# Kernel optimization log

Hardware: AMD Instinct MI355X
Metric: run time of the kernel (lower is better)

The kernel has to match this reference:

```python
import jax, jax.numpy as jnp
import numpy as np

D_MODEL = 2048
D_INNER = 2 * D_MODEL      # expand=2
D_STATE = 16
D_CONV = 4
DT_RANK = D_MODEL // 16    # ceil(2048/16)=128
BATCH, SEQLEN = 2, 1024


def setup_inputs() -> dict:
    key = jax.random.key(0)
    ks = jax.random.split(key, 10)
    s = 0.02
    inp = {
        "hidden_states": jax.random.normal(ks[0], (BATCH, SEQLEN, D_MODEL), jnp.float32),
        "in_proj_w": jax.random.normal(ks[1], (2 * D_INNER, D_MODEL), jnp.float32) * s,
        "conv_w": jax.random.normal(ks[2], (D_INNER, D_CONV), jnp.float32) * s,
        "conv_b": jax.random.normal(ks[3], (D_INNER,), jnp.float32) * s,
        "x_proj_w": jax.random.normal(ks[4], (DT_RANK + 2 * D_STATE, D_INNER), jnp.float32) * s,
        "dt_proj_w": jax.random.normal(ks[5], (D_INNER, DT_RANK), jnp.float32) * s,
        "dt_proj_b": jax.random.normal(ks[6], (D_INNER,), jnp.float32) * 0.1,
        "A_log": jnp.log(jnp.tile(jnp.arange(1, D_STATE + 1, dtype=jnp.float32), (D_INNER, 1))),
        "D": jnp.ones((D_INNER,), jnp.float32),
        "out_proj_w": jax.random.normal(ks[7], (D_MODEL, D_INNER), jnp.float32) * s,
    }
    return inp


def _mamba_forward(hidden_states, in_proj_w, conv_w, conv_b, x_proj_w,
                   dt_proj_w, dt_proj_b, A_log, D, out_proj_w):
    B, L, _ = hidden_states.shape
    # input projection -> x, z  (each [B, L, D_INNER])
    xz = jnp.einsum('bld,ed->ble', hidden_states, in_proj_w)
    x, z = jnp.split(xz, 2, axis=-1)
    # causal depthwise conv1d (kernel D_CONV) + SiLU
    x_pad = jnp.pad(x, ((0, 0), (D_CONV - 1, 0), (0, 0)))
    windows = jnp.stack([x_pad[:, k:k + L, :] for k in range(D_CONV)], axis=-1)  # [B,L,D,K]
    x_conv = jnp.einsum('bldk,dk->bld', windows, conv_w) + conv_b
    x_act = jax.nn.silu(x_conv)
    # data-dependent SSM parameters
    x_dbl = jnp.einsum('bld,ed->ble', x_act, x_proj_w)
    dt, Bc, Cc = jnp.split(x_dbl, [DT_RANK, DT_RANK + D_STATE], axis=-1)
    dt = jax.nn.softplus(jnp.einsum('blr,dr->bld', dt, dt_proj_w) + dt_proj_b)  # [B,L,D_INNER]
    A = -jnp.exp(A_log)  # [D_INNER, D_STATE]

    # selective scan over time (carry h: [B, D_INNER, D_STATE])
    def step(h, inp):
        x_t, dt_t, B_t, C_t = inp  # [B,D],[B,D],[B,N],[B,N]
        dA = jnp.exp(dt_t[:, :, None] * A[None])          # [B,D,N]
        dBx = dt_t[:, :, None] * B_t[:, None, :] * x_t[:, :, None]
        h = h * dA + dBx
        y = jnp.einsum('bdn,bn->bd', h, C_t)
        return h, y

    xs = (x_act.transpose(1, 0, 2), dt.transpose(1, 0, 2),
          Bc.transpose(1, 0, 2), Cc.transpose(1, 0, 2))
    h0 = jnp.zeros((B, D_INNER, D_STATE), x_act.dtype)
    _, ys = jax.lax.scan(step, h0, xs)          # [L,B,D_INNER]
    y = ys.transpose(1, 0, 2) + x_act * D       # skip connection D*x
    y = y * jax.nn.silu(z)                      # gating
    return jnp.einsum('bld,md->blm', y, out_proj_w)


def reference(hidden_states, in_proj_w, conv_w, conv_b, x_proj_w,
              dt_proj_w, dt_proj_b, A_log, D, out_proj_w):
    return _mamba_forward(hidden_states, in_proj_w, conv_w, conv_b, x_proj_w,
                          dt_proj_w, dt_proj_b, A_log, D, out_proj_w)
```

## Files before the change

kernel.cpp:

```cpp
#include <hip/hip_runtime.h>
#include <cstdint>
#include <cstddef>

#define D_MODEL 2048
#define D_INNER 4096
#define D_IN2   8192
#define D_STATE 16
#define D_CONVK 4
#define DT_RANK 128
#define BATCH   2
#define SEQLEN  1024
#define BL      (BATCH*SEQLEN)
#define XDBL_N  (DT_RANK + 2*D_STATE)
#define XPW_NPAD 256
#define XPROJ_SPLITS 8
#define OUT_SPLITS 2

#define NCHUNK  16
#define LCHUNK  (SEQLEN/NCHUNK)
#define CHW     (BATCH*D_INNER*D_STATE)

#define NB_HID   2048
#define NB_IPW   8192
#define NB_XPW   320
#define NB_XPWZ  192
#define NB_DTW   256
#define NB_OPW   4096
#define NB_XDBLZ 320

typedef short  s8v  __attribute__((ext_vector_type(8)));
typedef float  f4v  __attribute__((ext_vector_type(4)));

__device__ __forceinline__ float softplus_f(float v) {
    return (v > 20.f) ? v : log1pf(__expf(v));
}
__device__ __forceinline__ float silu_f(float v) {
    return v / (1.f + __expf(-v));
}
__device__ __forceinline__ float exp2_f(float x) {
    float r; asm("v_exp_f32 %0, %1" : "=v"(r) : "v"(x)); return r;
}
__device__ __forceinline__ float bf2f(short s) {
    return __uint_as_float(((uint32_t)(uint16_t)s) << 16);
}
__device__ __forceinline__ uint16_t f2bf(float f) {
    uint32_t u = __float_as_uint(f);
    return (uint16_t)((u + 0x7FFFu + ((u >> 16) & 1u)) >> 16);
}
__device__ __forceinline__ uint32_t packbf(float lo, float hi) {
    return ((uint32_t)f2bf(hi) << 16) | (uint32_t)f2bf(lo);
}
__device__ __forceinline__ float quad_sum(float p) {
    p += __int_as_float(__builtin_amdgcn_update_dpp(
            0, __float_as_int(p), 0xB1, 0xF, 0xF, true));
    p += __int_as_float(__builtin_amdgcn_update_dpp(
            0, __float_as_int(p), 0x4E, 0xF, 0xF, true));
    return p;
}

#define GLD16(gp, lp)                                                          \
    __builtin_amdgcn_global_load_lds(                                          \
        (const __attribute__((address_space(1))) void*)(gp),                   \
        (__attribute__((address_space(3))) void*)(lp), 16, 0, 0)

__global__ __launch_bounds__(256)
void k_cast_all(const float* __restrict__ s0, uint32_t* __restrict__ d0,
                const float* __restrict__ s1, uint32_t* __restrict__ d1,
                const float* __restrict__ s2, uint32_t* __restrict__ d2,
                const float* __restrict__ s3, uint32_t* __restrict__ d3,
                const float* __restrict__ s4, uint32_t* __restrict__ d4,
                uint32_t* __restrict__ z0, uint32_t* __restrict__ z1)
{
    int blk = blockIdx.x;
    const float* src = nullptr; uint32_t* dst; int base; int zero = 0;
    if      (blk < NB_HID) { src = s0; dst = d0; base = blk; }
    else if ((blk -= NB_HID)  < NB_IPW)  { src = s1; dst = d1; base = blk; }
    else if ((blk -= NB_IPW)  < NB_XPW)  { src = s2; dst = d2; base = blk; }
    else if ((blk -= NB_XPW)  < NB_XPWZ) { dst = z0; base = blk; zero = 1; }
    else if ((blk -= NB_XPWZ) < NB_DTW)  { src = s3; dst = d3; base = blk; }
    else if ((blk -= NB_DTW)  < NB_OPW)  { src = s4; dst = d4; base = blk; }
    else                                 { dst = z1; base = blk - NB_OPW; zero = 1; }
    const int i = base * 256 + threadIdx.x;
    if (zero) { ((uint4*)dst)[i] = make_uint4(0u, 0u, 0u, 0u); return; }
    const float4 a = ((const float4*)src)[i * 2];
    const float4 b = ((const float4*)src)[i * 2 + 1];
    uint4 o;
    o.x = packbf(a.x, a.y); o.y = packbf(a.z, a.w);
    o.z = packbf(b.x, b.y); o.w = packbf(b.z, b.w);
    ((uint4*)dst)[i] = o;
}

__global__ __launch_bounds__(512, 2)
void k_gemm_inproj(const short* __restrict__ A, const short* __restrict__ W,
                   short* __restrict__ C)
{
    constexpr int LDA = D_MODEL;
    constexpr int LDC = D_IN2;
    constexpr int NT  = D_MODEL / 64;

    __shared__ __align__(16) short smem[65536];

    const int tid = threadIdx.x;
    const int w   = tid >> 6;
    const int L   = tid & 63;
    const int bm  = blockIdx.y * 256;
    const int bn  = blockIdx.x * 256;

    const int srow = tid >> 2;
    const int g    = ((tid & 3) - (tid >> 3)) & 3;
    const short* Ag0 = A + (size_t)(bm + srow) * LDA + g * 8;
    const short* Ag1 = Ag0 + (size_t)128 * LDA;
    const short* Wg0 = W + (size_t)(bn + srow) * LDA + g * 8;
    const short* Wg1 = Wg0 + (size_t)128 * LDA;
    const int wofs = w * 512;

#define STG_A(t_, kh_) do {                                                    \
        GLD16(Ag0 + (size_t)(t_) * 64 + (kh_) * 32,                            \
              smem + (((t_) & 1) * 16384 + (kh_) * 8192 + wofs));              \
        GLD16(Ag1 + (size_t)(t_) * 64 + (kh_) * 32,                            \
              smem + (((t_) & 1) * 16384 + (kh_) * 8192 + 4096 + wofs));       \
    } while (0)
#define STG_B(t_, kh_) do {                                                    \
        GLD16(Wg0 + (size_t)(t_) * 64 + (kh_) * 32,                            \
              smem + (32768 + ((t_) & 1) * 16384 + (kh_) * 8192 + wofs));      \
        GLD16(Wg1 + (size_t)(t_) * 64 + (kh_) * 32,                            \
              smem + (32768 + ((t_) & 1) * 16384 + (kh_) * 8192 + 4096 + wofs));\
    } while (0)

    const int wm = w >> 2;
    const int wn = w & 3;
    const int cl = L & 15;
    const int qd = L >> 4;
    const int slot  = (qd + (cl >> 1)) & 3;
    const int abase = (wm * 128 + cl) * 32 + slot * 8;
    const int bbase = (wn * 64 + cl) * 32 + slot * 8;

    f4v acc[8][4];
#pragma unroll
    for (int i = 0; i < 8; i++)
#pragma unroll
        for (int j = 0; j < 4; j++) acc[i][j] = (f4v){0.f, 0.f, 0.f, 0.f};

#define LDS8(p) (*(const s8v*)(p))
#define MF(m_, n_, aa_, bb_)                                                   \
    acc[m_][n_] = __builtin_amdgcn_mfma_f32_16x16x32_bf16(                     \
        aa_, bb_, acc[m_][n_], 0, 0, 0)
#define MF16(m0_)                                                              \
    MF(m0_ + 0, 0, a0, b0); MF(m0_ + 1, 0, a1, b0);                            \
    MF(m0_ + 2, 0, a2, b0); MF(m0_ + 3, 0, a3, b0);                            \
    MF(m0_ + 0, 1, a0, b1); MF(m0_ + 1, 1, a1, b1);                            \
    MF(m0_ + 2, 1, a2, b1); MF(m0_ + 3, 1, a3, b1);                            \
    MF(m0_ + 0, 2, a0, b2); MF(m0_ + 1, 2, a1, b2);                            \
    MF(m0_ + 2, 2, a2, b2); MF(m0_ + 3, 2, a3, b2);                            \
    MF(m0_ + 0, 3, a0, b3); MF(m0_ + 1, 3, a1, b3);                            \
    MF(m0_ + 2, 3, a2, b3); MF(m0_ + 3, 3, a3, b3)
#define PH_SYNC() do {                                                         \
        __builtin_amdgcn_s_barrier();                                          \
        asm volatile("s_waitcnt lgkmcnt(0)" ::: "memory");                     \
        __builtin_amdgcn_sched_barrier(0);                                     \
    } while (0)

    STG_A(0, 0); STG_B(0, 0);
    __builtin_amdgcn_sched_barrier(0);
    STG_A(0, 1); STG_B(0, 1);
    __builtin_amdgcn_sched_barrier(0);
    STG_A(1, 0); STG_B(1, 0);
    asm volatile("s_waitcnt vmcnt(4)" ::: "memory");
    __builtin_amdgcn_s_barrier();

#pragma unroll 2
    for (int t = 0; t < NT; ++t) {
        const short* pA = smem + (t & 1) * 16384;
        const short* pB = smem + 32768 + (t & 1) * 16384;
        s8v a0, a1, a2, a3, b0, b1, b2, b3;

        a0 = LDS8(pA + abase);        a1 = LDS8(pA + abase + 512);
        a2 = LDS8(pA + abase + 1024); a3 = LDS8(pA + abase + 1536);
        b0 = LDS8(pB + bbase);        b1 = LDS8(pB + bbase + 512);
        b2 = LDS8(pB + bbase + 1024); b3 = LDS8(pB + bbase + 1536);
        if (t + 1 < NT) STG_A(t + 1, 1);
        PH_SYNC();
        __builtin_amdgcn_s_setprio(1);
        MF16(0);
        __builtin_amdgcn_s_setprio(0);
        __builtin_amdgcn_s_barrier();

        a0 = LDS8(pA + abase + 2048); a1 = LDS8(pA + abase + 2560);
        a2 = LDS8(pA + abase + 3072); a3 = LDS8(pA + abase + 3584);
        if (t + 1 < NT) STG_B(t + 1, 1);
        PH_SYNC();
        __builtin_amdgcn_s_setprio(1);
        MF16(4);
        __builtin_amdgcn_s_setprio(0);
        __builtin_amdgcn_s_barrier();

        a0 = LDS8(pA + 8192 + abase);        a1 = LDS8(pA + 8192 + abase + 512);
        a2 = LDS8(pA + 8192 + abase + 1024); a3 = LDS8(pA + 8192 + abase + 1536);
        b0 = LDS8(pB + 8192 + bbase);        b1 = LDS8(pB + 8192 + bbase + 512);
        b2 = LDS8(pB + 8192 + bbase + 1024); b3 = LDS8(pB + 8192 + bbase + 1536);
        if (t + 2 < NT) STG_A(t + 2, 0);
        PH_SYNC();
        __builtin_amdgcn_s_setprio(1);
        MF16(0);
        __builtin_amdgcn_s_setprio(0);
        __builtin_amdgcn_s_barrier();

        a0 = LDS8(pA + 8192 + abase + 2048); a1 = LDS8(pA + 8192 + abase + 2560);
        a2 = LDS8(pA + 8192 + abase + 3072); a3 = LDS8(pA + 8192 + abase + 3584);
        if (t + 2 < NT) STG_B(t + 2, 0);
        PH_SYNC();
        __builtin_amdgcn_s_setprio(1);
        MF16(4);
        __builtin_amdgcn_s_setprio(0);
        if (t < NT - 2) asm volatile("s_waitcnt vmcnt(4)" ::: "memory");
        else            asm volatile("s_waitcnt vmcnt(0)" ::: "memory");
        __builtin_amdgcn_s_barrier();
    }
#undef MF16
#undef MF
#undef LDS8
#undef STG_A
#undef STG_B
#undef PH_SYNC

    {
        ushort (*sC)[256] = (ushort(*)[256])smem;
#pragma unroll
        for (int mt = 0; mt < 8; mt++)
#pragma unroll
            for (int nt = 0; nt < 4; nt++)
#pragma unroll
                for (int r = 0; r < 4; r++)
                    sC[wm * 128 + mt * 16 + qd * 4 + r][wn * 64 + nt * 16 + cl] =
                        (ushort)f2bf(acc[mt][nt][r]);
        asm volatile("s_waitcnt lgkmcnt(0)" ::: "memory");
        __builtin_amdgcn_s_barrier();
#pragma unroll
        for (int it = 0; it < 16; it++) {
            const int idx = it * 512 + tid;
            const int row = idx >> 5;
            const int c8s = (idx & 31) * 8;
            *(uint4*)&C[(size_t)(bm + row) * LDC + bn + c8s] =
                *(const uint4*)&sC[row][c8s];
        }
    }
}

template<int EPI>
__device__ __forceinline__
void gemm_body(const short* __restrict__ A, int lda,
               const short* __restrict__ W, int ldw,
               void* __restrict__ Cv, int ldc, int M, int kchunk)
{
    constexpr int SMEM_BYTES = (EPI == 0) ? 33792 : 32768;
    __shared__ __align__(16) char smem[SMEM_BYTES];
    short* sA = (short*)smem;
    short* sW = (short*)(smem + 16384);

    const int tid = threadIdx.x;
    const int w   = tid >> 6;
    const int L   = tid & 63;
    const int bm  = blockIdx.y * 128;
    const int bn  = blockIdx.x * 128;
    const int k0  = blockIdx.z * kchunk;

    const int rsub = L >> 3;
    const int c8   = (((L & 7) - rsub) & 7) * 8;
    const short* Ag[4]; const short* Wg[4];
#pragma unroll
    for (int j = 0; j < 4; j++) {
        Ag[j] = A + (size_t)(bm + w * 32 + j * 8 + rsub) * lda + c8 + k0;
        Wg[j] = W + (size_t)(bn + w * 32 + j * 8 + rsub) * ldw + c8 + k0;
    }

    const int wm = (w >> 1) * 64;
    const int wn = (w & 1) * 64;
    const int cl = L & 15;
    const int qd = L >> 4;

    f4v acc[4][4];
#pragma unroll
    for (int i = 0; i < 4; i++)
#pragma unroll
        for (int j = 0; j < 4; j++) acc[i][j] = (f4v){0.f, 0.f, 0.f, 0.f};

    for (int k = 0; k < kchunk; k += 64) {
#pragma unroll
        for (int j = 0; j < 4; j++)
            GLD16(Ag[j] + k, &sA[(w * 32 + j * 8) * 64]);
#pragma unroll
        for (int j = 0; j < 4; j++)
            GLD16(Wg[j] + k, &sW[(w * 32 + j * 8) * 64]);
        __syncthreads();
#pragma unroll
        for (int kk = 0; kk < 2; kk++) {
            const int sl = ((kk * 4 + qd + cl) & 7) * 8;
            s8v a[4], b[4];
#pragma unroll
            for (int mt = 0; mt < 4; mt++)
                a[mt] = *(const s8v*)&sA[(wm + mt * 16 + cl) * 64 + sl];
#pragma unroll
            for (int nt = 0; nt < 4; nt++)
                b[nt] = *(const s8v*)&sW[(wn + nt * 16 + cl) * 64 + sl];
#pragma unroll
            for (int mt = 0; mt < 4; mt++)
#pragma unroll
                for (int nt = 0; nt < 4; nt++)
                    acc[mt][nt] = __builtin_amdgcn_mfma_f32_16x16x32_bf16(
                        a[mt], b[nt], acc[mt][nt], 0, 0, 0);
        }
        __syncthreads();
    }

    if constexpr (EPI == 0) {
        float (*sC)[132] = (float(*)[132])smem;
        float* Cf = (float*)Cv + (size_t)blockIdx.z * M * ldc;
#pragma unroll
        for (int half = 0; half < 2; half++) {
            __syncthreads();
            if (wm == half * 64) {
#pragma unroll
                for (int mt = 0; mt < 4; mt++)
#pragma unroll
                    for (int nt = 0; nt < 4; nt++)
#pragma unroll
                        for (int r = 0; r < 4; r++)
                            sC[mt * 16 + qd * 4 + r][wn + nt * 16 + cl] =
                                acc[mt][nt][r];
            }
            __syncthreads();
#pragma unroll
            for (int it = 0; it < 8; it++) {
                const int f4  = it * 256 + tid;
                const int row = f4 >> 5;
                const int c4  = (f4 & 31) * 4;
                const float4 v = *(const float4*)&sC[row][c4];
                *(float4*)&Cf[(size_t)(bm + half * 64 + row) * ldc + bn + c4] = v;
            }
        }
    } else {
        float* Cf = (float*)Cv;
#pragma unroll
        for (int mt = 0; mt < 4; mt++) {
            const int row0 = bm + wm + mt * 16 + qd * 4;
#pragma unroll
            for (int nt = 0; nt < 4; nt++) {
                const int col = bn + wn + nt * 16 + cl;
                if (col >= XDBL_N) continue;
#pragma unroll
                for (int r = 0; r < 4; r++)
                    atomicAdd(&Cf[(size_t)(row0 + r) * ldc + col], acc[mt][nt][r]);
            }
        }
    }
}

__global__ __launch_bounds__(256)
void k_gemm_xproj(const short* A, const short* W, float* C)
{ gemm_body<3>(A, D_INNER, W, D_INNER, C, XDBL_N, BL, D_INNER / XPROJ_SPLITS); }

__global__ __launch_bounds__(256)
void k_gemm_outproj(const short* A, const short* W, float* C)
{ gemm_body<0>(A, D_INNER, W, D_INNER, C, D_MODEL, BL, D_INNER / OUT_SPLITS); }

__global__ __launch_bounds__(256)
void k_gemm_dt(const float* __restrict__ Af, const short* __restrict__ W,
               float* __restrict__ C)
{
    __shared__ __align__(16) char smem[65536];
    short* sA = (short*)smem;
    short* sW = (short*)(smem + 32768);

    const int tid = threadIdx.x;
    const int w   = tid >> 6;
    const int L   = tid & 63;
    const int bm  = blockIdx.y * 128;
    const int bn  = blockIdx.x * 128;

#pragma unroll
    for (int ci = 0; ci < 8; ci++) {
        const int c_lin = tid * 8 + ci;
        const int r = c_lin >> 4;
        const int c = c_lin & 15;
        const float* src = Af + (size_t)(bm + r) * XDBL_N + c * 8;
        const float4 u = *(const float4*)src;
        const float4 v = *(const float4*)(src + 4);
        const int half = c >> 3, cc = c & 7;
        const int slot = (cc + r) & 7;
        uint4 o;
        o.x = packbf(u.x, u.y); o.y = packbf(u.z, u.w);
        o.z = packbf(v.x, v.y); o.w = packbf(v.z, v.w);
        *(uint4*)&sA[half * 8192 + r * 64 + slot * 8] = o;
    }
    const int rsub = L >> 3;
    const int c8   = (((L & 7) - rsub) & 7) * 8;
#pragma unroll
    for (int half = 0; half < 2; half++)
#pragma unroll
        for (int j = 0; j < 4; j++)
            GLD16(W + (size_t)(bn + w * 32 + j * 8 + rsub) * DT_RANK + half * 64 + c8,
                  &sW[half * 8192 + (w * 32 + j * 8) * 64]);
    __syncthreads();

    const int wm = (w >> 1) * 64;
    const int wn = (w & 1) * 64;
    const int cl = L & 15;
    const int qd = L >> 4;

    f4v acc[4][4];
#pragma unroll
    for (int i = 0; i < 4; i++)
#pragma unroll
        for (int j = 0; j < 4; j++) acc[i][j] = (f4v){0.f, 0.f, 0.f, 0.f};

#pragma unroll
    for (int ks = 0; ks < 4; ks++) {
        const int half = ks >> 1;
        const int sl = (((ks & 1) * 4 + qd + cl) & 7) * 8;
        s8v a[4], b[4];
#pragma unroll
        for (int mt = 0; mt < 4; mt++)
            a[mt] = *(const s8v*)&sA[half * 8192 + (wm + mt * 16 + cl) * 64 + sl];
#pragma unroll
        for (int nt = 0; nt < 4; nt++)
            b[nt] = *(const s8v*)&sW[half * 8192 + (wn + nt * 16 + cl) * 64 + sl];
#pragma unroll
        for (int mt = 0; mt < 4; mt++)
#pragma unroll
            for (int nt = 0; nt < 4; nt++)
                acc[mt][nt] = __builtin_amdgcn_mfma_f32_16x16x32_bf16(
                    a[mt], b[nt], acc[mt][nt], 0, 0, 0);
    }

    __syncthreads();
    float (*sC)[132] = (float(*)[132])smem;
#pragma unroll
    for (int half = 0; half < 2; half++) {
        __syncthreads();
        if (wm == half * 64) {
#pragma unroll
            for (int mt = 0; mt < 4; mt++)
#pragma unroll
                for (int nt = 0; nt < 4; nt++)
#pragma unroll
                    for (int r = 0; r < 4; r++)
                        sC[mt * 16 + qd * 4 + r][wn + nt * 16 + cl] =
                            acc[mt][nt][r];
        }
        __syncthreads();
#pragma unroll
        for (int it = 0; it < 8; it++) {
            const int f4  = it * 256 + tid;
            const int row = f4 >> 5;
            const int c4  = (f4 & 31) * 4;
            const float4 v = *(const float4*)&sC[row][c4];
            *(float4*)&C[(size_t)(bm + half * 64 + row) * D_INNER + bn + c4] = v;
        }
    }
}

__global__ __launch_bounds__(256)
void k_reduce_out(const float* __restrict__ P, float* __restrict__ out)
{
    const int i = blockIdx.x * 256 + threadIdx.x;
    const float4 a = ((const float4*)P)[i];
    const float4 b = ((const float4*)(P + (size_t)BL * D_MODEL))[i];
    ((float4*)out)[i] = make_float4(a.x + b.x, a.y + b.y, a.z + b.z, a.w + b.w);
}

__global__ __launch_bounds__(256)
void k_conv(const short* __restrict__ xz_bf, const float* __restrict__ cw,
            const float* __restrict__ cb, short* __restrict__ x_bf)
{
    const int idx = blockIdx.x * 256 + threadIdx.x;
    const int d  = idx & (D_INNER - 1);
    const int bl = idx >> 12;
    const int l  = bl & (SEQLEN - 1);
    const int b  = bl >> 10;
    const short* xb = xz_bf + (size_t)b * SEQLEN * D_IN2 + d;
    float acc = cb[d];
#pragma unroll
    for (int k = 0; k < D_CONVK; k++) {
        const int ll = l + k - (D_CONVK - 1);
        if (ll >= 0) acc = fmaf(bf2f(xb[(size_t)ll * D_IN2]), cw[d * D_CONVK + k], acc);
    }
    x_bf[idx] = (short)f2bf(silu_f(acc));
}

__global__ __launch_bounds__(256)
void k_scan_p1(const short* __restrict__ x_bf, const float* __restrict__ dtr,
               const float* __restrict__ dtb, const float* __restrict__ xdbl,
               const float* __restrict__ A_log,
               float* __restrict__ h_end, float* __restrict__ Pprod)
{
    const int c   = blockIdx.y;
    const int ch0 = blockIdx.x * 64;
    const int b   = ch0 >> 12;
    const int d0  = ch0 & (D_INNER - 1);
    const int tid = threadIdx.x;
    const int g   = tid >> 2;
    const int q   = tid & 3;
    const int d   = d0 + g;

    const float LOG2E = 1.44269504f;
    const float4 Al = *(const float4*)&A_log[(d << 4) + (q << 2)];
    float An[4] = {-__expf(Al.x) * LOG2E, -__expf(Al.y) * LOG2E,
                   -__expf(Al.z) * LOG2E, -__expf(Al.w) * LOG2E};
    float h[4]  = {0.f, 0.f, 0.f, 0.f};
    float Pp[4] = {1.f, 1.f, 1.f, 1.f};

    __shared__ float s_x [16][68];
    __shared__ float s_dt[16][68];
    __shared__ float s_B [16][20];

    const int lt  = tid >> 4;
    const int ld4 = (tid & 15) * 4;
    const float4 bb = *(const float4*)&dtb[d0 + ld4];

    for (int sub = 0; sub < LCHUNK / 16; sub++) {
        const int l0 = c * LCHUNK + sub * 16;
        const size_t bl = (size_t)(b * SEQLEN + l0 + lt);
        __syncthreads();
        {
            const short4 sx = *(const short4*)&x_bf[bl * D_INNER + d0 + ld4];
            const float4 dv = *(const float4*)&dtr[bl * D_INNER + d0 + ld4];
            *(float4*)&s_x [lt][ld4] =
                make_float4(bf2f(sx.x), bf2f(sx.y), bf2f(sx.z), bf2f(sx.w));
            *(float4*)&s_dt[lt][ld4] = make_float4(
                softplus_f(dv.x + bb.x), softplus_f(dv.y + bb.y),
                softplus_f(dv.z + bb.z), softplus_f(dv.w + bb.w));
            if (tid < 64) {
                const int t2 = tid >> 2, k = (tid & 3) * 4;
                const size_t bl2 = (size_t)(b * SEQLEN + l0 + t2);
                *(float4*)&s_B[t2][k] =
                    *(const float4*)&xdbl[bl2 * XDBL_N + DT_RANK + k];
            }
        }
        __syncthreads();
#pragma unroll
        for (int t = 0; t < 16; t++) {
            const float xv  = s_x [t][g];
            const float dtv = s_dt[t][g];
            const float4 Bq = *(const float4*)&s_B[t][q * 4];
            const float Bv[4] = {Bq.x, Bq.y, Bq.z, Bq.w};
            const float dtx = dtv * xv;
#pragma unroll
            for (int j = 0; j < 4; j++) {
                const float dA = exp2_f(dtv * An[j]);
                h[j]  = fmaf(h[j], dA, dtx * Bv[j]);
                Pp[j] *= dA;
            }
        }
    }
    const size_t i0 = (size_t)c * CHW + (((size_t)(b * D_INNER + d)) << 4) + (q << 2);
    *(float4*)&h_end[i0] = make_float4(h[0], h[1], h[2], h[3]);
    *(float4*)&Pprod[i0] = make_float4(Pp[0], Pp[1], Pp[2], Pp[3]);
}

__global__ __launch_bounds__(256)
void k_scan_p3(const short* __restrict__ x_bf, short* __restrict__ y_bf,
               const float* __restrict__ dtr, const float* __restrict__ dtb,
               const float* __restrict__ xdbl,
               const short* __restrict__ xz_bf, const float* __restrict__ A_log,
               const float* __restrict__ Dvec,
               const float* __restrict__ h_end, const float* __restrict__ Pbuf)
{
    const int c   = blockIdx.y;
    const int ch0 = blockIdx.x * 64;
    const int b   = ch0 >> 12;
    const int d0  = ch0 & (D_INNER - 1);
    const int tid = threadIdx.x;
    const int g   = tid >> 2;
    const int q   = tid & 3;
    const int d   = d0 + g;

    const float LOG2E = 1.44269504f;
    const float4 Al = *(const float4*)&A_log[(d << 4) + (q << 2)];
    float An[4] = {-__expf(Al.x) * LOG2E, -__expf(Al.y) * LOG2E,
                   -__expf(Al.z) * LOG2E, -__expf(Al.w) * LOG2E};
    const float Dd = Dvec[d];

    float h[4] = {0.f, 0.f, 0.f, 0.f};
    const size_t base = (((size_t)(b * D_INNER + d)) << 4) + (q << 2);
    {
        int j = 0;
        for (; j + 4 <= c; j += 4) {
            float4 he[4], Pq[4];
#pragma unroll
            for (int u = 0; u < 4; u++) {
                he[u] = *(const float4*)&h_end[(size_t)(j + u) * CHW + base];
                Pq[u] = *(const float4*)&Pbuf [(size_t)(j + u) * CHW + base];
            }
#pragma unroll
            for (int u = 0; u < 4; u++) {
                h[0] = fmaf(Pq[u].x, h[0], he[u].x);
                h[1] = fmaf(Pq[u].y, h[1], he[u].y);
                h[2] = fmaf(Pq[u].z, h[2], he[u].z);
                h[3] = fmaf(Pq[u].w, h[3], he[u].w);
            }
        }
        for (; j < c; j++) {
            const float4 he = *(const float4*)&h_end[(size_t)j * CHW + base];
            const float4 Pq = *(const float4*)&Pbuf [(size_t)j * CHW + base];
            h[0] = fmaf(Pq.x, h[0], he.x);
            h[1] = fmaf(Pq.y, h[1], he.y);
            h[2] = fmaf(Pq.z, h[2], he.z);
            h[3] = fmaf(Pq.w, h[3], he.w);
        }
    }

    __shared__ float s_x [16][68];
    __shared__ float s_dt[16][68];
    __shared__ float s_z [16][68];
    __shared__ float s_B [16][20];
    __shared__ float s_C [16][20];

    const int lt  = tid >> 4;
    const int ld4 = (tid & 15) * 4;
    const float4 bb = *(const float4*)&dtb[d0 + ld4];

    for (int sub = 0; sub < LCHUNK / 16; sub++) {
        const int l0 = c * LCHUNK + sub * 16;
        const size_t bl = (size_t)(b * SEQLEN + l0 + lt);
        __syncthreads();
        {
            const short4 sx = *(const short4*)&x_bf[bl * D_INNER + d0 + ld4];
            const float4 dv = *(const float4*)&dtr[bl * D_INNER + d0 + ld4];
            const short4 zv = *(const short4*)&xz_bf[bl * D_IN2 + D_INNER + d0 + ld4];
            *(float4*)&s_x [lt][ld4] =
                make_float4(bf2f(sx.x), bf2f(sx.y), bf2f(sx.z), bf2f(sx.w));
            *(float4*)&s_dt[lt][ld4] = make_float4(
                softplus_f(dv.x + bb.x), softplus_f(dv.y + bb.y),
                softplus_f(dv.z + bb.z), softplus_f(dv.w + bb.w));
            *(float4*)&s_z [lt][ld4] = make_float4(
                silu_f(bf2f(zv.x)), silu_f(bf2f(zv.y)),
                silu_f(bf2f(zv.z)), silu_f(bf2f(zv.w)));
            if (tid < 128) {
                const int t2 = (tid & 63) >> 2, k = (tid & 3) * 4;
                const size_t bl2 = (size_t)(b * SEQLEN + l0 + t2);
                const int off = (tid < 64) ? 0 : D_STATE;
                const float4 v =
                    *(const float4*)&xdbl[bl2 * XDBL_N + DT_RANK + off + k];
                if (tid < 64) *(float4*)&s_B[t2][k] = v;
                else          *(float4*)&s_C[t2][k] = v;
            }
        }
        __syncthreads();
        const size_t orow = (size_t)(b * SEQLEN + l0);
#pragma unroll
        for (int t = 0; t < 16; t++) {
            const float xv  = s_x [t][g];
            const float dtv = s_dt[t][g];
            const float4 Bq = *(const float4*)&s_B[t][q * 4];
            const float4 Cq = *(const float4*)&s_C[t][q * 4];
            const float Bv[4] = {Bq.x, Bq.y, Bq.z, Bq.w};
            const float Cv[4] = {Cq.x, Cq.y, Cq.z, Cq.w};
            const float dtx = dtv * xv;
            float p = 0.f;
#pragma unroll
            for (int j = 0; j < 4; j++) {
                const float dA = exp2_f(dtv * An[j]);
                h[j] = fmaf(h[j], dA, dtx * Bv[j]);
                p = fmaf(h[j], Cv[j], p);
            }
            p = quad_sum(p);
            if (q == 0) {
                const float yv = fmaf(xv, Dd, p) * s_z[t][g];
                y_bf[(orow + t) * D_INNER + d] = (short)f2bf(yv);
            }
        }
    }
}

extern "C" void kernel_launch(void* const* d_in, const int* in_sizes, int n_in,
                              void* d_out, int out_size, void* d_ws, size_t ws_size,
                              hipStream_t stream)
{
    const float* hidden     = (const float*)d_in[0];
    const float* in_proj_w  = (const float*)d_in[1];
    const float* conv_w     = (const float*)d_in[2];
    const float* conv_b     = (const float*)d_in[3];
    const float* x_proj_w   = (const float*)d_in[4];
    const float* dt_proj_w  = (const float*)d_in[5];
    const float* dt_proj_b  = (const float*)d_in[6];
    const float* A_log      = (const float*)d_in[7];
    const float* Dvec       = (const float*)d_in[8];
    const float* out_proj_w = (const float*)d_in[9];
    float* out = (float*)d_out;

    const size_t MB = 1ull << 20;
    char* ws = (char*)d_ws;
    short* xz_bf   = (short*)(ws);
    short* x_bf    = (short*)(ws + 32 * MB);
    short* ipw_bf  = (short*)(ws + 48 * MB);
    short* y_bf    = (short*)(ws + 48 * MB);
    float* h_end   = (float*)(ws + 64 * MB);
    float* Pbuf    = (float*)(ws + 72 * MB);
    short* hid_bf  = (short*)(ws + 80 * MB);
    short* opw_bf  = (short*)(ws + 88 * MB);
    float* dt_raw  = (float*)(ws + 104 * MB);
    float* op_part = (float*)(ws + 104 * MB);
    short* xpw_bf  = (short*)(ws + 136 * MB);
    short* dtw_bf  = (short*)(ws + 138 * MB);
    float* xdbl_f  = (float*)(ws + 139 * MB);

    const dim3 blk(256);

    k_cast_all<<<dim3(NB_HID + NB_IPW + NB_XPW + NB_XPWZ + NB_DTW + NB_OPW + NB_XDBLZ),
                blk, 0, stream>>>(
        hidden, (uint32_t*)hid_bf, in_proj_w, (uint32_t*)ipw_bf,
        x_proj_w, (uint32_t*)xpw_bf, dt_proj_w, (uint32_t*)dtw_bf,
        out_proj_w, (uint32_t*)opw_bf,
        (uint32_t*)(xpw_bf + (size_t)XDBL_N * D_INNER),
        (uint32_t*)xdbl_f);

    k_gemm_inproj<<<dim3(D_IN2 / 256, BL / 256), dim3(512), 0, stream>>>(
        hid_bf, ipw_bf, xz_bf);

    k_conv<<<dim3((BL * D_INNER) / 256), blk, 0, stream>>>(
        xz_bf, conv_w, conv_b, x_bf);

    k_gemm_xproj<<<dim3(XPW_NPAD / 128, BL / 128, XPROJ_SPLITS), blk, 0, stream>>>(
        x_bf, xpw_bf, xdbl_f);

    k_gemm_dt<<<dim3(D_INNER / 128, BL / 128), blk, 0, stream>>>(
        xdbl_f, dtw_bf, dt_raw);

    k_scan_p1<<<dim3(BATCH * D_INNER / 64, NCHUNK - 1), blk, 0, stream>>>(
        x_bf, dt_raw, dt_proj_b, xdbl_f, A_log, h_end, Pbuf);
    k_scan_p3<<<dim3(BATCH * D_INNER / 64, NCHUNK), blk, 0, stream>>>(
        x_bf, y_bf, dt_raw, dt_proj_b, xdbl_f, xz_bf, A_log, Dvec, h_end, Pbuf);

    k_gemm_outproj<<<dim3(D_MODEL / 128, BL / 128, OUT_SPLITS), blk, 0, stream>>>(
        y_bf, opw_bf, op_part);
    k_reduce_out<<<dim3(BL * D_MODEL / 4 / 256), blk, 0, stream>>>(op_part, out);
}
```

Before: 441.8 us.

## Port out_proj to 256x256 pipelined MFMA kernel with 4-way split-K; widen scan blocks

Replaces the generic 128x128 out_proj GEMM with a 512-thread 256x256 tile kernel that uses the same double-buffered direct-to-LDS pipeline as in_proj. It switches to 4-way split-K, with partials stored in workspace regions that are free by then, and reduces them in a 4-input reduce kernel. The scan kernels now handle 128 channels per 512-thread block instead of 64 per 256. The aim is better MFMA utilisation and data reuse in out_proj, at the cost of more partial-sum traffic and fewer blocks in the grid.

Result: slower. 452.1 us (+2.3%).

```diff
diff --git a/kernel.cpp b/kernel.cpp
--- a/kernel.cpp
+++ b/kernel.cpp
@@ -14,7 +14,7 @@
 #define XDBL_N  (DT_RANK + 2*D_STATE)
 #define XPW_NPAD 256
 #define XPROJ_SPLITS 8
-#define OUT_SPLITS 2
+#define OUT_SPLITS 4
 
 #define NCHUNK  16
 #define LCHUNK  (SEQLEN/NCHUNK)
@@ -216,44 +216,207 @@
         else            asm volatile("s_waitcnt vmcnt(0)" ::: "memory");
         __builtin_amdgcn_s_barrier();
     }
+
+    {
+        ushort (*sC)[256] = (ushort(*)[256])smem;
+#pragma unroll
+        for (int mt = 0; mt < 8; mt++)
+#pragma unroll
+            for (int nt = 0; nt < 4; nt++)
+#pragma unroll
+                for (int r = 0; r < 4; r++)
+                    sC[wm * 128 + mt * 16 + qd * 4 + r][wn * 64 + nt * 16 + cl] =
+                        (ushort)f2bf(acc[mt][nt][r]);
+        asm volatile("s_waitcnt lgkmcnt(0)" ::: "memory");
+        __builtin_amdgcn_s_barrier();
+#pragma unroll
+        for (int it = 0; it < 16; it++) {
+            const int idx = it * 512 + tid;
+            const int row = idx >> 5;
+            const int c8s = (idx & 31) * 8;
+            *(uint4*)&C[(size_t)(bm + row) * LDC + bn + c8s] =
+                *(const uint4*)&sC[row][c8s];
+        }
+    }
 #undef MF16
 #undef MF
 #undef LDS8
 #undef STG_A
 #undef STG_B
 #undef PH_SYNC
-
-    {
-        ushort (*sC)[256] = (ushort(*)[256])smem;
-#pragma unroll
-        for (int mt = 0; mt < 8; mt++)
-#pragma unroll
-            for (int nt = 0; nt < 4; nt++)
-#pragma unroll
-                for (int r = 0; r < 4; r++)
-                    sC[wm * 128 + mt * 16 + qd * 4 + r][wn * 64 + nt * 16 + cl] =
-                        (ushort)f2bf(acc[mt][nt][r]);
+}
+
+__global__ __launch_bounds__(512, 2)
+void k_gemm_outproj(const short* __restrict__ A, const short* __restrict__ W,
+                    float* __restrict__ P0, float* __restrict__ P3)
+{
+    constexpr int LDA = D_INNER;
+    constexpr int LDC = D_MODEL;
+    constexpr int KCH = D_INNER / OUT_SPLITS;
+    constexpr int NT  = KCH / 64;
+
+    __shared__ __align__(16) short smem[65536];
+
+    const int tid = threadIdx.x;
+    const int w   = tid >> 6;
+    const int L   = tid & 63;
+    const int bm  = blockIdx.y * 256;
+    const int bn  = blockIdx.x * 256;
+    const int k0  = blockIdx.z * KCH;
+
+    const int srow = tid >> 2;
+    const int g    = ((tid & 3) - (tid >> 3)) & 3;
+    const short* Ag0 = A + (size_t)(bm + srow) * LDA + k0 + g * 8;
+    const short* Ag1 = Ag0 + (size_t)128 * LDA;
+    const short* Wg0 = W + (size_t)(bn + srow) * LDA + k0 + g * 8;
+    const short* Wg1 = Wg0 + (size_t)128 * LDA;
+    const int wofs = w * 512;
+
+#define STG_A(t_, kh_) do {                                                    \
+        GLD16(Ag0 + (size_t)(t_) * 64 + (kh_) * 32,                            \
+              smem + (((t_) & 1) * 16384 + (kh_) * 8192 + wofs));              \
+        GLD16(Ag1 + (size_t)(t_) * 64 + (kh_) * 32,                            \
+              smem + (((t_) & 1) * 16384 + (kh_) * 8192 + 4096 + wofs));       \
+    } while (0)
+#define STG_B(t_, kh_) do {                                                    \
+        GLD16(Wg0 + (size_t)(t_) * 64 + (kh_) * 32,                            \
+              smem + (32768 + ((t_) & 1) * 16384 + (kh_) * 8192 + wofs));      \
+        GLD16(Wg1 + (size_t)(t_) * 64 + (kh_) * 32,                            \
+              smem + (32768 + ((t_) & 1) * 16384 + (kh_) * 8192 + 4096 + wofs));\
+    } while (0)
+
+    const int wm = w >> 2;
+    const int wn = w & 3;
+    const int cl = L & 15;
+    const int qd = L >> 4;
+    const int slot  = (qd + (cl >> 1)) & 3;
+    const int abase = (wm * 128 + cl) * 32 + slot * 8;
+    const int bbase = (wn * 64 + cl) * 32 + slot * 8;
+
+    f4v acc[8][4];
+#pragma unroll
+    for (int i = 0; i < 8; i++)
+#pragma unroll
+        for (int j = 0; j < 4; j++) acc[i][j] = (f4v){0.f, 0.f, 0.f, 0.f};
+
+#define LDS8(p) (*(const s8v*)(p))
+#define MF(m_, n_, aa_, bb_)                                                   \
+    acc[m_][n_] = __builtin_amdgcn_mfma_f32_16x16x32_bf16(                     \
+        aa_, bb_, acc[m_][n_], 0, 0, 0)
+#define MF16(m0_)                                                              \
+    MF(m0_ + 0, 0, a0, b0); MF(m0_ + 1, 0, a1, b0);                            \
+    MF(m0_ + 2, 0, a2, b0); MF(m0_ + 3, 0, a3, b0);                            \
+    MF(m0_ + 0, 1, a0, b1); MF(m0_ + 1, 1, a1, b1);                            \
+    MF(m0_ + 2, 1, a2, b1); MF(m0_ + 3, 1, a3, b1);                            \
+    MF(m0_ + 0, 2, a0, b2); MF(m0_ + 1, 2, a1, b2);                            \
+    MF(m0_ + 2, 2, a2, b2); MF(m0_ + 3, 2, a3, b2);                            \
+    MF(m0_ + 0, 3, a0, b3); MF(m0_ + 1, 3, a1, b3);                            \
+    MF(m0_ + 2, 3, a2, b3); MF(m0_ + 3, 3, a3, b3)
+#define PH_SYNC() do {                                                         \
+        __builtin_amdgcn_s_barrier();                                          \
+        asm volatile("s_waitcnt lgkmcnt(0)" ::: "memory");                     \
+        __builtin_amdgcn_sched_barrier(0);                                     \
+    } while (0)
+
+    STG_A(0, 0); STG_B(0, 0);
+    __builtin_amdgcn_sched_barrier(0);
+    STG_A(0, 1); STG_B(0, 1);
+    __builtin_amdgcn_sched_barrier(0);
+    STG_A(1, 0); STG_B(1, 0);
+    asm volatile("s_waitcnt vmcnt(4)" ::: "memory");
+    __builtin_amdgcn_s_barrier();
+
+#pragma unroll 2
+    for (int t = 0; t < NT; ++t) {
+        const short* pA = smem + (t & 1) * 16384;
+        const short* pB = smem + 32768 + (t & 1) * 16384;
+        s8v a0, a1, a2, a3, b0, b1, b2, b3;
+
+        a0 = LDS8(pA + abase);        a1 = LDS8(pA + abase + 512);
+        a2 = LDS8(pA + abase + 1024); a3 = LDS8(pA + abase + 1536);
+        b0 = LDS8(pB + bbase);        b1 = LDS8(pB + bbase + 512);
+        b2 = LDS8(pB + bbase + 1024); b3 = LDS8(pB + bbase + 1536);
+        if (t + 1 < NT) STG_A(t + 1, 1);
+        PH_SYNC();
+        __builtin_amdgcn_s_setprio(1);
+        MF16(0);
+        __builtin_amdgcn_s_setprio(0);
+        __builtin_amdgcn_s_barrier();
+
+        a0 = LDS8(pA + abase + 2048); a1 = LDS8(pA + abase + 2560);
+        a2 = LDS8(pA + abase + 3072); a3 = LDS8(pA + abase + 3584);
+        if (t + 1 < NT) STG_B(t + 1, 1);
+        PH_SYNC();
+        __builtin_amdgcn_s_setprio(1);
+        MF16(4);
+        __builtin_amdgcn_s_setprio(0);
+        __builtin_amdgcn_s_barrier();
+
+        a0 = LDS8(pA + 8192 + abase);        a1 = LDS8(pA + 8192 + abase + 512);
+        a2 = LDS8(pA + 8192 + abase + 1024); a3 = LDS8(pA + 8192 + abase + 1536);
+        b0 = LDS8(pB + 8192 + bbase);        b1 = LDS8(pB + 8192 + bbase + 512);
+        b2 = LDS8(pB + 8192 + bbase + 1024); b3 = LDS8(pB + 8192 + bbase + 1536);
+        if (t + 2 < NT) STG_A(t + 2, 0);
+        PH_SYNC();
+        __builtin_amdgcn_s_setprio(1);
+        MF16(0);
+        __builtin_amdgcn_s_setprio(0);
+        __builtin_amdgcn_s_barrier();
+
+        a0 = LDS8(pA + 8192 + abase + 2048); a1 = LDS8(pA + 8192 + abase + 2560);
+        a2 = LDS8(pA + 8192 + abase + 3072); a3 = LDS8(pA + 8192 + abase + 3584);
+        if (t + 2 < NT) STG_B(t + 2, 0);
+        PH_SYNC();
+        __builtin_amdgcn_s_setprio(1);
+        MF16(4);
+        __builtin_amdgcn_s_setprio(0);
+        if (t < NT - 2) asm volatile("s_waitcnt vmcnt(4)" ::: "memory");
+        else            asm volatile("s_waitcnt vmcnt(0)" ::: "memory");
+        __builtin_amdgcn_s_barrier();
+    }
+#undef MF16
+#undef MF
+#undef LDS8
+#undef STG_A
+#undef STG_B
+#undef PH_SYNC
+
+    float* Cf = (blockIdx.z < 3)
+              ? P0 + (size_t)blockIdx.z * BL * LDC
+              : P3;
+    float (*sCf)[256] = (float(*)[256])smem;
+#pragma unroll
+    for (int half = 0; half < 2; half++) {
+        if (half) __builtin_amdgcn_s_barrier();
+        if (wm == half) {
+#pragma unroll
+            for (int mt = 0; mt < 8; mt++)
+#pragma unroll
+                for (int nt = 0; nt < 4; nt++)
+#pragma unroll
+                    for (int r = 0; r < 4; r++)
+                        sCf[mt * 16 + qd * 4 + r][wn * 64 + nt * 16 + cl] =
+                            acc[mt][nt][r];
+        }
         asm volatile("s_waitcnt lgkmcnt(0)" ::: "memory");
         __builtin_amdgcn_s_barrier();
 #pragma unroll
         for (int it = 0; it < 16; it++) {
             const int idx = it * 512 + tid;
-            const int row = idx >> 5;
-            const int c8s = (idx & 31) * 8;
-            *(uint4*)&C[(size_t)(bm + row) * LDC + bn + c8s] =
-                *(const uint4*)&sC[row][c8s];
-        }
-    }
-}
-
-template<int EPI>
+            const int row = idx >> 6;
+            const int c4  = (idx & 63) * 4;
+            *(float4*)&Cf[(size_t)(bm + half * 128 + row) * LDC + bn + c4] =
+                *(const float4*)&sCf[row][c4];
+        }
+    }
+}
+
 __device__ __forceinline__
-void gemm_body(const short* __restrict__ A, int lda,
-               const short* __restrict__ W, int ldw,
-               void* __restrict__ Cv, int ldc, int M, int kchunk)
-{
-    constexpr int SMEM_BYTES = (EPI == 0) ? 33792 : 32768;
-    __shared__ __align__(16) char smem[SMEM_BYTES];
+void gemm_body3(const short* __restrict__ A, int lda,
+                const short* __restrict__ W, int ldw,
+                float* __restrict__ Cf, int ldc, int kchunk)
+{
+    __shared__ __align__(16) char smem[32768];
     short* sA = (short*)smem;
     short* sW = (short*)(smem + 16384);
 
@@ -312,56 +475,23 @@
         __syncthreads();
     }
 
-    if constexpr (EPI == 0) {
-        float (*sC)[132] = (float(*)[132])smem;
-        float* Cf = (float*)Cv + (size_t)blockIdx.z * M * ldc;
-#pragma unroll
-        for (int half = 0; half < 2; half++) {
-            __syncthreads();
-            if (wm == half * 64) {
-#pragma unroll
-                for (int mt = 0; mt < 4; mt++)
-#pragma unroll
-                    for (int nt = 0; nt < 4; nt++)
-#pragma unroll
-                        for (int r = 0; r < 4; r++)
-                            sC[mt * 16 + qd * 4 + r][wn + nt * 16 + cl] =
-                                acc[mt][nt][r];
-            }
-            __syncthreads();
-#pragma unroll
-            for (int it = 0; it < 8; it++) {
-                const int f4  = it * 256 + tid;
-                const int row = f4 >> 5;
-                const int c4  = (f4 & 31) * 4;
-                const float4 v = *(const float4*)&sC[row][c4];
-                *(float4*)&Cf[(size_t)(bm + half * 64 + row) * ldc + bn + c4] = v;
-            }
-        }
-    } else {
-        float* Cf = (float*)Cv;
-#pragma unroll
-        for (int mt = 0; mt < 4; mt++) {
-            const int row0 = bm + wm + mt * 16 + qd * 4;
-#pragma unroll
-            for (int nt = 0; nt < 4; nt++) {
-                const int col = bn + wn + nt * 16 + cl;
-                if (col >= XDBL_N) continue;
-#pragma unroll
-                for (int r = 0; r < 4; r++)
-                    atomicAdd(&Cf[(size_t)(row0 + r) * ldc + col], acc[mt][nt][r]);
-            }
+#pragma unroll
+    for (int mt = 0; mt < 4; mt++) {
+        const int row0 = bm + wm + mt * 16 + qd * 4;
+#pragma unroll
+        for (int nt = 0; nt < 4; nt++) {
+            const int col = bn + wn + nt * 16 + cl;
+            if (col >= XDBL_N) continue;
+#pragma unroll
+            for (int r = 0; r < 4; r++)
+                atomicAdd(&Cf[(size_t)(row0 + r) * ldc + col], acc[mt][nt][r]);
         }
     }
 }
 
 __global__ __launch_bounds__(256)
 void k_gemm_xproj(const short* A, const short* W, float* C)
-{ gemm_body<3>(A, D_INNER, W, D_INNER, C, XDBL_N, BL, D_INNER / XPROJ_SPLITS); }
-
-__global__ __launch_bounds__(256)
-void k_gemm_outproj(const short* A, const short* W, float* C)
-{ gemm_body<0>(A, D_INNER, W, D_INNER, C, D_MODEL, BL, D_INNER / OUT_SPLITS); }
+{ gemm_body3(A, D_INNER, W, D_INNER, C, XDBL_N, D_INNER / XPROJ_SPLITS); }
 
 __global__ __launch_bounds__(256)
 void k_gemm_dt(const float* __restrict__ Af, const short* __restrict__ W,
@@ -460,12 +590,19 @@
 }
 
 __global__ __launch_bounds__(256)
-void k_reduce_out(const float* __restrict__ P, float* __restrict__ out)
+void k_reduce_out(const float* __restrict__ P0, const float* __restrict__ P3,
+                  float* __restrict__ out)
 {
     const int i = blockIdx.x * 256 + threadIdx.x;
-    const float4 a = ((const float4*)P)[i];
-    const float4 b = ((const float4*)(P + (size_t)BL * D_MODEL))[i];
-    ((float4*)out)[i] = make_float4(a.x + b.x, a.y + b.y, a.z + b.z, a.w + b.w);
+    const size_t S = (size_t)BL * D_MODEL / 4;
+    const float4 a = ((const float4*)P0)[i];
+    const float4 b = ((const float4*)P0)[i + S];
+    const float4 c = ((const float4*)P0)[i + 2 * S];
+    const float4 d = ((const float4*)P3)[i];
+    ((float4*)out)[i] = make_float4(((a.x + b.x) + c.x) + d.x,
+                                    ((a.y + b.y) + c.y) + d.y,
+                                    ((a.z + b.z) + c.z) + d.z,
+                                    ((a.w + b.w) + c.w) + d.w);
 }
 
 __global__ __launch_bounds__(256)
@@ -487,14 +624,14 @@
     x_bf[idx] = (short)f2bf(silu_f(acc));
 }
 
-__global__ __launch_bounds__(256)
+__global__ __launch_bounds__(512)
 void k_scan_p1(const short* __restrict__ x_bf, const float* __restrict__ dtr,
                const float* __restrict__ dtb, const float* __restrict__ xdbl,
                const float* __restrict__ A_log,
                float* __restrict__ h_end, float* __restrict__ Pprod)
 {
     const int c   = blockIdx.y;
-    const int ch0 = blockIdx.x * 64;
+    const int ch0 = blockIdx.x * 128;
     const int b   = ch0 >> 12;
     const int d0  = ch0 & (D_INNER - 1);
     const int tid = threadIdx.x;
@@ -509,12 +646,12 @@
     float h[4]  = {0.f, 0.f, 0.f, 0.f};
     float Pp[4] = {1.f, 1.f, 1.f, 1.f};
 
-    __shared__ float s_x [16][68];
-    __shared__ float s_dt[16][68];
+    __shared__ float s_x [16][132];
+    __shared__ float s_dt[16][132];
     __shared__ float s_B [16][20];
 
-    const int lt  = tid >> 4;
-    const int ld4 = (tid & 15) * 4;
+    const int lt  = tid >> 5;
+    const int ld4 = (tid & 31) * 4;
     const float4 bb = *(const float4*)&dtb[d0 + ld4];
 
     for (int sub = 0; sub < LCHUNK / 16; sub++) {
@@ -557,7 +694,7 @@
     *(float4*)&Pprod[i0] = make_float4(Pp[0], Pp[1], Pp[2], Pp[3]);
 }
 
-__global__ __launch_bounds__(256)
+__global__ __launch_bounds__(512)
 void k_scan_p3(const short* __restrict__ x_bf, short* __restrict__ y_bf,
                const float* __restrict__ dtr, const float* __restrict__ dtb,
                const float* __restrict__ xdbl,
@@ -566,7 +703,7 @@
                const float* __restrict__ h_end, const float* __restrict__ Pbuf)
 {
     const int c   = blockIdx.y;
-    const int ch0 = blockIdx.x * 64;
+    const int ch0 = blockIdx.x * 128;
     const int b   = ch0 >> 12;
     const int d0  = ch0 & (D_INNER - 1);
     const int tid = threadIdx.x;
@@ -609,14 +746,14 @@
         }
     }
 
-    __shared__ float s_x [16][68];
-    __shared__ float s_dt[16][68];
-    __shared__ float s_z [16][68];
+    __shared__ float s_x [16][132];
+    __shared__ float s_dt[16][132];
+    __shared__ float s_z [16][132];
     __shared__ float s_B [16][20];
     __shared__ float s_C [16][20];
 
-    const int lt  = tid >> 4;
-    const int ld4 = (tid & 15) * 4;
+    const int lt  = tid >> 5;
+    const int ld4 = (tid & 31) * 4;
     const float4 bb = *(const float4*)&dtb[d0 + ld4];
 
     for (int sub = 0; sub < LCHUNK / 16; sub++) {
@@ -699,10 +836,11 @@
     short* hid_bf  = (short*)(ws + 80 * MB);
     short* opw_bf  = (short*)(ws + 88 * MB);
     float* dt_raw  = (float*)(ws + 104 * MB);
-    float* op_part = (float*)(ws + 104 * MB);
     short* xpw_bf  = (short*)(ws + 136 * MB);
     short* dtw_bf  = (short*)(ws + 138 * MB);
     float* xdbl_f  = (float*)(ws + 139 * MB);
+    float* op_P0   = (float*)(ws);
+    float* op_P3   = (float*)(ws + 64 * MB);
 
     const dim3 blk(256);
 
@@ -726,12 +864,13 @@
     k_gemm_dt<<<dim3(D_INNER / 128, BL / 128), blk, 0, stream>>>(
         xdbl_f, dtw_bf, dt_raw);
 
-    k_scan_p1<<<dim3(BATCH * D_INNER / 64, NCHUNK - 1), blk, 0, stream>>>(
+    k_scan_p1<<<dim3(BATCH * D_INNER / 128, NCHUNK - 1), dim3(512), 0, stream>>>(
         x_bf, dt_raw, dt_proj_b, xdbl_f, A_log, h_end, Pbuf);
-    k_scan_p3<<<dim3(BATCH * D_INNER / 64, NCHUNK), blk, 0, stream>>>(
+    k_scan_p3<<<dim3(BATCH * D_INNER / 128, NCHUNK), dim3(512), 0, stream>>>(
         x_bf, y_bf, dt_raw, dt_proj_b, xdbl_f, xz_bf, A_log, Dvec, h_end, Pbuf);
 
-    k_gemm_outproj<<<dim3(D_MODEL / 128, BL / 128, OUT_SPLITS), blk, 0, stream>>>(
-        y_bf, opw_bf, op_part);
-    k_reduce_out<<<dim3(BL * D_MODEL / 4 / 256), blk, 0, stream>>>(op_part, out);
-}
+    k_gemm_outproj<<<dim3(D_MODEL / 256, BL / 256, OUT_SPLITS), dim3(512), 0, stream>>>(
+        y_bf, opw_bf, op_P0, op_P3);
+    k_reduce_out<<<dim3(BL * D_MODEL / 4 / 256), blk, 0, stream>>>(
+        op_P0, op_P3, out);
+}
```
